# Performance work log

Hardware: AMD Instinct MI355X
Metric: run time of the kernel (lower is better)

## Reference

```python
import jax, jax.numpy as jnp
import numpy as np
from jax import lax

# WGS-84 gravity constants (matching sgp4 getgravconst('wgs-84'))
TWOPI = 2.0 * np.pi
MU = 398600.5            # km^3/s^2
RE = 6378.137            # km
XKE = 60.0 / float(np.sqrt(RE ** 3 / MU))
J2 = 0.00108262998905
J3 = -0.00000253215306
J4 = -0.00000161098761
J3OJ2 = J3 / J2
X2O3 = 2.0 / 3.0
TEMP4 = 1.5e-12


def _sgp4(sgp4_params, t):
    """Vectorized near-earth SGP4: sgp4init + propagate, per-satellite elementwise."""
    n_kozai = sgp4_params[..., 0]   # rad/min (Kozai mean motion)
    ecco    = sgp4_params[..., 1]
    inclo   = sgp4_params[..., 2]
    nodeo   = sgp4_params[..., 3]
    argpo   = sgp4_params[..., 4]
    mo      = sgp4_params[..., 5]
    bstar   = sgp4_params[..., 6]

    # ---------------- sgp4init (near-earth branch) ----------------
    ss = 78.0 / RE + 1.0
    qzms2t = ((120.0 - 78.0) / RE) ** 4
    eccsq = ecco * ecco
    omeosq = 1.0 - eccsq
    rteosq = jnp.sqrt(omeosq)
    cosio = jnp.cos(inclo)
    cosio2 = cosio * cosio
    ak = (XKE / n_kozai) ** X2O3
    d1 = 0.75 * J2 * (3.0 * cosio2 - 1.0) / (rteosq * omeosq)
    del_ = d1 / (ak * ak)
    adel = ak * (1.0 - del_ * del_ - del_ * (1.0 / 3.0 + 134.0 * del_ * del_ / 81.0))
    del_ = d1 / (adel * adel)
    no_unkozai = n_kozai / (1.0 + del_)
    ao = (XKE / no_unkozai) ** X2O3
    sinio = jnp.sin(inclo)
    po = ao * omeosq
    con42 = 1.0 - 5.0 * cosio2
    con41 = -con42 - 2.0 * cosio2
    posq = po * po
    rp = ao * (1.0 - ecco)

    isimp = rp < (220.0 / RE + 1.0)
    perige = (rp - 1.0) * RE
    sfour_low = jnp.where(perige < 98.0, 20.0, perige - 78.0)
    qzms24_low = ((120.0 - sfour_low) / RE) ** 4
    low = perige < 156.0
    sfour = jnp.where(low, sfour_low / RE + 1.0, ss)
    qzms24 = jnp.where(low, qzms24_low, qzms2t)

    pinvsq = 1.0 / posq
    tsi = 1.0 / (ao - sfour)
    eta = ao * ecco * tsi
    etasq = eta * eta
    eeta = ecco * eta
    psisq = jnp.abs(1.0 - etasq)
    coef = qzms24 * tsi ** 4
    coef1 = coef / psisq ** 3.5
    cc2 = coef1 * no_unkozai * (ao * (1.0 + 1.5 * etasq + eeta * (4.0 + etasq))
          + 0.375 * J2 * tsi / psisq * con41 * (8.0 + 3.0 * etasq * (8.0 + etasq)))
    cc1 = bstar * cc2
    safe_e = jnp.maximum(ecco, 1e-4)
    cc3 = jnp.where(ecco > 1e-4, -2.0 * coef * tsi * J3OJ2 * no_unkozai * sinio / safe_e, 0.0)
    x1mth2 = 1.0 - cosio2
    cc4 = 2.0 * no_unkozai * coef1 * ao * omeosq * (
        eta * (2.0 + 0.5 * etasq) + ecco * (0.5 + 2.0 * etasq)
        - J2 * tsi / (ao * psisq) * (-3.0 * con41 * (1.0 - 2.0 * eeta + etasq * (1.5 - 0.5 * eeta))
        + 0.75 * x1mth2 * (2.0 * etasq - eeta * (1.0 + etasq)) * jnp.cos(2.0 * argpo)))
    cc5 = 2.0 * coef1 * ao * omeosq * (1.0 + 2.75 * (etasq + eeta) + eeta * etasq)
    cosio4 = cosio2 * cosio2
    temp1 = 1.5 * J2 * pinvsq * no_unkozai
    temp2 = 0.5 * temp1 * J2 * pinvsq
    temp3 = -0.46875 * J4 * pinvsq * pinvsq * no_unkozai
    mdot = no_unkozai + 0.5 * temp1 * rteosq * con41 + 0.0625 * temp2 * rteosq * (13.0 - 78.0 * cosio2 + 137.0 * cosio4)
    argpdot = (-0.5 * temp1 * con42 + 0.0625 * temp2 * (7.0 - 114.0 * cosio2 + 395.0 * cosio4)
               + temp3 * (3.0 - 36.0 * cosio2 + 49.0 * cosio4))
    xhdot1 = -temp1 * cosio
    nodedot = xhdot1 + (0.5 * temp2 * (4.0 - 19.0 * cosio2) + 2.0 * temp3 * (3.0 - 7.0 * cosio2)) * cosio
    omgcof = bstar * cc3 * jnp.cos(argpo)
    safe_eeta = jnp.where(jnp.abs(eeta) > 1e-12, eeta, 1.0)
    xmcof = jnp.where(ecco > 1e-4, -X2O3 * coef * bstar / safe_eeta, 0.0)
    nodecf = 3.5 * omeosq * xhdot1 * cc1
    t2cof = 1.5 * cc1
    denom = jnp.where(jnp.abs(1.0 + cosio) > 1.5e-12, 1.0 + cosio, TEMP4)
    xlcof = -0.25 * J3OJ2 * sinio * (3.0 + 5.0 * cosio) / denom
    aycof = -0.5 * J3OJ2 * sinio
    delmo = (1.0 + eta * jnp.cos(mo)) ** 3
    sinmao = jnp.sin(mo)
    x7thm1 = 7.0 * cosio2 - 1.0
    # non-isimp (drag) higher order coefficients
    cc1sq = cc1 * cc1
    d2 = 4.0 * ao * tsi * cc1sq
    tmp = d2 * tsi * cc1 / 3.0
    d3 = (17.0 * ao + sfour) * tmp
    d4 = 0.5 * tmp * ao * tsi * (221.0 * ao + 31.0 * sfour) * cc1
    t3cof = d2 + 2.0 * cc1sq
    t4cof = 0.25 * (3.0 * d3 + cc1 * (12.0 * d2 + 10.0 * cc1sq))
    t5cof = 0.2 * (3.0 * d4 + 12.0 * cc1 * d3 + 6.0 * d2 * d2 + 15.0 * cc1sq * (2.0 * d2 + cc1sq))

    # ---------------- propagation (sgp4) ----------------
    xmdf = mo + mdot * t
    argpdf = argpo + argpdot * t
    nodedf = nodeo + nodedot * t
    t2 = t * t
    nodem = nodedf + nodecf * t2
    tempa0 = 1.0 - cc1 * t
    tempe0 = bstar * cc4 * t
    templ0 = t2cof * t2
    delomg = omgcof * t
    delm = xmcof * ((1.0 + eta * jnp.cos(xmdf)) ** 3 - delmo)
    per = delomg + delm
    mm = jnp.where(isimp, xmdf, xmdf + per)
    argpm = jnp.where(isimp, argpdf, argpdf - per)
    t3 = t2 * t
    t4 = t3 * t
    tempa = jnp.where(isimp, tempa0, tempa0 - d2 * t2 - d3 * t3 - d4 * t4)
    tempe = jnp.where(isimp, tempe0, tempe0 + bstar * cc5 * (jnp.sin(mm) - sinmao))
    templ = jnp.where(isimp, templ0, templ0 + t3cof * t3 + t4cof * t4 + t5cof * t4 * t)

    am = ((XKE / no_unkozai) ** X2O3) * tempa * tempa
    nm = XKE / am ** 1.5
    em = jnp.maximum(ecco - tempe, 1e-6)
    mm = mm + no_unkozai * templ
    xlm = mm + argpm + nodem
    nodem = jnp.mod(nodem, TWOPI)
    argpm = jnp.mod(argpm, TWOPI)
    xlm = jnp.mod(xlm, TWOPI)
    mm = jnp.mod(xlm - argpm - nodem, TWOPI)

    sinim = jnp.sin(inclo)
    cosim = jnp.cos(inclo)
    axnl = em * jnp.cos(argpm)
    tinv = 1.0 / (am * (1.0 - em * em))
    aynl = em * jnp.sin(argpm) + tinv * aycof
    xl = mm + argpm + nodem + tinv * xlcof * axnl
    u = jnp.mod(xl - nodem, TWOPI)

    # Newton-Raphson Kepler solve, fixed 10 iterations, clamped step (as in sgp4)
    def kepler_step(_, eo1):
        s = jnp.sin(eo1)
        c = jnp.cos(eo1)
        tem5 = (u - aynl * c + axnl * s - eo1) / (1.0 - c * axnl - s * aynl)
        return eo1 + jnp.clip(tem5, -0.95, 0.95)
    eo1 = lax.fori_loop(0, 10, kepler_step, u)

    sineo1 = jnp.sin(eo1)
    coseo1 = jnp.cos(eo1)
    ecose = axnl * coseo1 + aynl * sineo1
    esine = axnl * sineo1 - aynl * coseo1
    el2 = axnl * axnl + aynl * aynl
    pl = am * (1.0 - el2)
    rl = am * (1.0 - ecose)
    rdotl = jnp.sqrt(am) * esine / rl
    rvdotl = jnp.sqrt(pl) / rl
    betal = jnp.sqrt(1.0 - el2)
    tq = esine / (1.0 + betal)
    sinu = am / rl * (sineo1 - aynl - axnl * tq)
    cosu = am / rl * (coseo1 - axnl + aynl * tq)
    su = jnp.arctan2(sinu, cosu)
    sin2u = 2.0 * cosu * sinu
    cos2u = 1.0 - 2.0 * sinu * sinu
    pli = 1.0 / pl
    tb = 0.5 * J2 * pli
    tc = tb * pli
    # short-period periodics
    mrt = rl * (1.0 - 1.5 * tc * betal * con41) + 0.5 * tb * x1mth2 * cos2u
    su = su - 0.25 * tc * x7thm1 * sin2u
    xnode = nodem + 1.5 * tc * cosim * sin2u
    xinc = inclo + 1.5 * tc * cosim * sinim * cos2u
    mvt = rdotl - nm * tb * x1mth2 * sin2u / XKE
    rvdot = rvdotl + nm * tb * (x1mth2 * cos2u + 1.5 * con41) / XKE

    sinsu = jnp.sin(su)
    cossu = jnp.cos(su)
    snod = jnp.sin(xnode)
    cnod = jnp.cos(xnode)
    sini = jnp.sin(xinc)
    cosi = jnp.cos(xinc)
    xmx = -snod * cosi
    xmy = cnod * cosi
    uvec = jnp.stack([xmx * sinsu + cnod * cossu,
                      xmy * sinsu + snod * cossu,
                      sini * sinsu], axis=-1)             # (N, 3)
    vvec = jnp.stack([xmx * cossu - cnod * sinsu,
                      xmy * cossu - snod * sinsu,
                      sini * cossu], axis=-1)             # (N, 3)

    vkps = RE * XKE / 60.0
    pos = (mrt * RE)[..., None] * uvec                     # km, TEME
    vel = vkps * (mvt[..., None] * uvec + rvdot[..., None] * vvec)  # km/s
    return pos, vel


def setup_inputs() -> dict:
    key = jax.random.key(0)
    N = 1_000_000
    k1, k2 = jax.random.split(key)
    uu = jax.random.uniform(k1, (N, 7), dtype=jnp.float32)
    n = 0.045 + 0.015 * uu[:, 0]          # rad/min, period 105-140 min (near-earth)
    e = 0.001 + 0.019 * uu[:, 1]          # low eccentricity, perigee above Earth
    i = np.pi * uu[:, 2]
    raan = TWOPI * uu[:, 3]
    argp = TWOPI * uu[:, 4]
    ma = TWOPI * uu[:, 5]
    bstar = 1e-4 * (uu[:, 6] - 0.5)
    sgp4_params = jnp.stack([n, e, i, raan, argp, ma, bstar], axis=-1)
    t_minutes = jax.random.uniform(k2, (N,), dtype=jnp.float32) * 1440.0
    return {"sgp4_params": sgp4_params, "t_minutes": t_minutes}


def reference(sgp4_params, t_minutes):
    pos, vel = _sgp4(sgp4_params, t_minutes)
    return pos, vel
```

## Files before the change

kernel.cpp:

```cpp
#include <hip/hip_runtime.h>
#include <math.h>


namespace {
constexpr double RE_D   = 6378.137;
constexpr double MU_D   = 398600.5;
constexpr double J2_D   = 0.00108262998905;
constexpr double J3_D   = -0.00000253215306;
constexpr double J4_D   = -0.00000161098761;
constexpr double TWOPI_D = 6.28318530717958647692528676655900577;
}

#define FC(x) ((float)(x))

__device__ __forceinline__ float mod_twopi(float x) {
    const float TP = FC(TWOPI_D);
    float r = fmodf(x, TP);
    return (r < 0.0f) ? r + TP : r;
}

__global__ __launch_bounds__(256) void sgp4_kernel(
    const float* __restrict__ prm,
    const float* __restrict__ tmin,
    float* __restrict__ out,
    int N)
{
    const int i = blockIdx.x * blockDim.x + threadIdx.x;
    if (i >= N) return;

    const float RE    = FC(RE_D);
    const float XKE   = FC(60.0 / __builtin_sqrt(RE_D * RE_D * RE_D / MU_D));
    const float J2    = FC(J2_D);
    const float J4    = FC(J4_D);
    const float J3OJ2 = FC(J3_D / J2_D);
    const float X2O3  = FC(2.0 / 3.0);
    const float SS    = FC(78.0 / RE_D + 1.0);
    const float QZMS2T = FC(((120.0 - 78.0) / RE_D) * ((120.0 - 78.0) / RE_D) *
                            ((120.0 - 78.0) / RE_D) * ((120.0 - 78.0) / RE_D));
    const float TEMP4 = 1.5e-12f;
    const float VKPS  = FC(RE_D * (60.0 / __builtin_sqrt(RE_D * RE_D * RE_D / MU_D)) / 60.0);

    const float* p = prm + (size_t)i * 7;
    const float n_kozai = p[0];
    const float ecco    = p[1];
    const float inclo   = p[2];
    const float nodeo   = p[3];
    const float argpo   = p[4];
    const float mo      = p[5];
    const float bstar   = p[6];
    const float t       = tmin[i];

    const float eccsq  = ecco * ecco;
    const float omeosq = 1.0f - eccsq;
    const float rteosq = sqrtf(omeosq);
    const float cosio  = cosf(inclo);
    const float sinio  = sinf(inclo);
    const float cosio2 = cosio * cosio;

    const float ak   = __powf(XKE / n_kozai, X2O3);
    const float d1   = 0.75f * J2 * (3.0f * cosio2 - 1.0f) / (rteosq * omeosq);
    float del_ = d1 / (ak * ak);
    const float adel = ak * (1.0f - del_ * del_ - del_ * (1.0f / 3.0f + 134.0f * del_ * del_ / 81.0f));
    del_ = d1 / (adel * adel);
    const float no_unkozai = n_kozai / (1.0f + del_);
    const float ao   = __powf(XKE / no_unkozai, X2O3);
    const float po   = ao * omeosq;
    const float con42 = 1.0f - 5.0f * cosio2;
    const float con41 = -con42 - 2.0f * cosio2;
    const float posq = po * po;
    const float rp   = ao * (1.0f - ecco);

    const bool  isimp = rp < (220.0f / RE + 1.0f);
    const float perige = (rp - 1.0f) * RE;
    const float sfour_low = (perige < 98.0f) ? 20.0f : (perige - 78.0f);
    float q24 = (120.0f - sfour_low) / RE;
    q24 = q24 * q24;
    q24 = q24 * q24;
    const bool  low    = perige < 156.0f;
    const float sfour  = low ? (sfour_low / RE + 1.0f) : SS;
    const float qzms24 = low ? q24 : QZMS2T;

    const float pinvsq = 1.0f / posq;
    const float tsi   = 1.0f / (ao - sfour);
    const float eta   = ao * ecco * tsi;
    const float etasq = eta * eta;
    const float eeta  = ecco * eta;
    const float psisq = fabsf(1.0f - etasq);
    const float tsi2  = tsi * tsi;
    const float coef  = qzms24 * (tsi2 * tsi2);
    const float coef1 = coef / (psisq * psisq * psisq * sqrtf(psisq));
    const float cc2 = coef1 * no_unkozai * (ao * (1.0f + 1.5f * etasq + eeta * (4.0f + etasq))
        + 0.375f * J2 * tsi / psisq * con41 * (8.0f + 3.0f * etasq * (8.0f + etasq)));
    const float cc1 = bstar * cc2;
    const float safe_e = fmaxf(ecco, 1e-4f);
    const float cc3 = (ecco > 1e-4f)
        ? (-2.0f * coef * tsi * J3OJ2 * no_unkozai * sinio / safe_e) : 0.0f;
    const float x1mth2 = 1.0f - cosio2;
    const float cc4 = 2.0f * no_unkozai * coef1 * ao * omeosq * (
        eta * (2.0f + 0.5f * etasq) + ecco * (0.5f + 2.0f * etasq)
        - J2 * tsi / (ao * psisq) * (-3.0f * con41 * (1.0f - 2.0f * eeta + etasq * (1.5f - 0.5f * eeta))
        + 0.75f * x1mth2 * (2.0f * etasq - eeta * (1.0f + etasq)) * __cosf(2.0f * argpo)));
    const float cc5 = 2.0f * coef1 * ao * omeosq * (1.0f + 2.75f * (etasq + eeta) + eeta * etasq);
    const float cosio4 = cosio2 * cosio2;
    const float temp1 = 1.5f * J2 * pinvsq * no_unkozai;
    const float temp2 = 0.5f * temp1 * J2 * pinvsq;
    const float temp3 = -0.46875f * J4 * pinvsq * pinvsq * no_unkozai;
    const float mdot = no_unkozai + 0.5f * temp1 * rteosq * con41
        + 0.0625f * temp2 * rteosq * (13.0f - 78.0f * cosio2 + 137.0f * cosio4);
    const float argpdot = -0.5f * temp1 * con42
        + 0.0625f * temp2 * (7.0f - 114.0f * cosio2 + 395.0f * cosio4)
        + temp3 * (3.0f - 36.0f * cosio2 + 49.0f * cosio4);
    const float xhdot1 = -temp1 * cosio;
    const float nodedot = xhdot1 + (0.5f * temp2 * (4.0f - 19.0f * cosio2)
        + 2.0f * temp3 * (3.0f - 7.0f * cosio2)) * cosio;
    const float omgcof = bstar * cc3 * __cosf(argpo);
    const float safe_eeta = (fabsf(eeta) > 1e-12f) ? eeta : 1.0f;
    const float xmcof = (ecco > 1e-4f) ? (-X2O3 * coef * bstar / safe_eeta) : 0.0f;
    const float nodecf = 3.5f * omeosq * xhdot1 * cc1;
    const float t2cof  = 1.5f * cc1;
    const float opc    = 1.0f + cosio;
    const float denom  = (fabsf(opc) > TEMP4) ? opc : TEMP4;
    const float xlcof  = -0.25f * J3OJ2 * sinio * (3.0f + 5.0f * cosio) / denom;
    const float aycof  = -0.5f * J3OJ2 * sinio;
    const float cmo    = __cosf(mo);
    const float dmt    = 1.0f + eta * cmo;
    const float delmo  = dmt * dmt * dmt;
    const float sinmao = __sinf(mo);
    const float x7thm1 = 7.0f * cosio2 - 1.0f;
    const float cc1sq = cc1 * cc1;
    const float d2 = 4.0f * ao * tsi * cc1sq;
    const float dtmp = d2 * tsi * cc1 / 3.0f;
    const float d3 = (17.0f * ao + sfour) * dtmp;
    const float d4 = 0.5f * dtmp * ao * tsi * (221.0f * ao + 31.0f * sfour) * cc1;
    const float t3cof = d2 + 2.0f * cc1sq;
    const float t4cof = 0.25f * (3.0f * d3 + cc1 * (12.0f * d2 + 10.0f * cc1sq));
    const float t5cof = 0.2f * (3.0f * d4 + 12.0f * cc1 * d3 + 6.0f * d2 * d2
        + 15.0f * cc1sq * (2.0f * d2 + cc1sq));

    const float xmdf   = mo + mdot * t;
    const float argpdf = argpo + argpdot * t;
    const float nodedf = nodeo + nodedot * t;
    const float t2 = t * t;
    float nodem = nodedf + nodecf * t2;
    float tempa = 1.0f - cc1 * t;
    float tempe = bstar * cc4 * t;
    float templ = t2cof * t2;
    const float delomg = omgcof * t;
    const float cxm = 1.0f + eta * __cosf(xmdf);
    const float delm = xmcof * (cxm * cxm * cxm - delmo);
    const float per = delomg + delm;
    float mm    = isimp ? xmdf : (xmdf + per);
    float argpm = isimp ? argpdf : (argpdf - per);
    const float t3 = t2 * t;
    const float t4 = t3 * t;
    if (!isimp) {
        tempa = tempa - d2 * t2 - d3 * t3 - d4 * t4;
        tempe = tempe + bstar * cc5 * (__sinf(mm) - sinmao);
        templ = templ + t3cof * t3 + t4cof * t4 + t5cof * t4 * t;
    }

    const float am = ao * tempa * tempa;
    const float nm = XKE / (am * sqrtf(am));
    const float em = fmaxf(ecco - tempe, 1e-6f);
    mm = mm + no_unkozai * templ;
    float xlm = mm + argpm + nodem;
    nodem = mod_twopi(nodem);
    argpm = mod_twopi(argpm);
    xlm   = mod_twopi(xlm);
    mm    = mod_twopi(xlm - argpm - nodem);

    const float sinim = sinio;
    const float cosim = cosio;
    const float sargpm = __sinf(argpm);
    const float cargpm = __cosf(argpm);
    const float axnl = em * cargpm;
    const float tinv = 1.0f / (am * (1.0f - em * em));
    const float aynl = em * sargpm + tinv * aycof;
    const float xl = mm + argpm + nodem + tinv * xlcof * axnl;
    const float u = mod_twopi(xl - nodem);

    float eo1 = u;
#pragma unroll
    for (int k = 0; k < 10; ++k) {
        const float s = __sinf(eo1);
        const float c = __cosf(eo1);
        float tem5 = (u - aynl * c + axnl * s - eo1) / (1.0f - c * axnl - s * aynl);
        tem5 = fminf(fmaxf(tem5, -0.95f), 0.95f);
        eo1 += tem5;
    }

    const float sineo1 = __sinf(eo1);
    const float coseo1 = __cosf(eo1);
    const float ecose = axnl * coseo1 + aynl * sineo1;
    const float esine = axnl * sineo1 - aynl * coseo1;
    const float el2 = axnl * axnl + aynl * aynl;
    const float pl = am * (1.0f - el2);
    const float rl = am * (1.0f - ecose);
    const float rlinv = 1.0f / rl;
    const float rdotl = sqrtf(am) * esine * rlinv;
    const float rvdotl = sqrtf(pl) * rlinv;
    const float betal = sqrtf(1.0f - el2);
    const float tq = esine / (1.0f + betal);
    const float sinu = am * rlinv * (sineo1 - aynl - axnl * tq);
    const float cosu = am * rlinv * (coseo1 - axnl + aynl * tq);
    float su = atan2f(sinu, cosu);
    const float sin2u = 2.0f * cosu * sinu;
    const float cos2u = 1.0f - 2.0f * sinu * sinu;
    const float pli = 1.0f / pl;
    const float tb = 0.5f * J2 * pli;
    const float tc = tb * pli;
    const float mrt = rl * (1.0f - 1.5f * tc * betal * con41) + 0.5f * tb * x1mth2 * cos2u;
    su = su - 0.25f * tc * x7thm1 * sin2u;
    const float xnode = nodem + 1.5f * tc * cosim * sin2u;
    const float xinc = inclo + 1.5f * tc * cosim * sinim * cos2u;
    const float mvt = rdotl - nm * tb * x1mth2 * sin2u / XKE;
    const float rvdot = rvdotl + nm * tb * (x1mth2 * cos2u + 1.5f * con41) / XKE;

    const float sinsu = __sinf(su);
    const float cossu = __cosf(su);
    const float snod = __sinf(xnode);
    const float cnod = __cosf(xnode);
    const float sini = __sinf(xinc);
    const float cosi = __cosf(xinc);
    const float xmx = -snod * cosi;
    const float xmy = cnod * cosi;
    const float ux = xmx * sinsu + cnod * cossu;
    const float uy = xmy * sinsu + snod * cossu;
    const float uz = sini * sinsu;
    const float vx = xmx * cossu - cnod * sinsu;
    const float vy = xmy * cossu - snod * sinsu;
    const float vz = sini * cossu;

    const float mr = mrt * RE;
    const size_t base = (size_t)3 * (size_t)i;
    float* __restrict__ vout = out + (size_t)3 * (size_t)N;
    out[base + 0] = mr * ux;
    out[base + 1] = mr * uy;
    out[base + 2] = mr * uz;
    vout[base + 0] = VKPS * (mvt * ux + rvdot * vx);
    vout[base + 1] = VKPS * (mvt * uy + rvdot * vy);
    vout[base + 2] = VKPS * (mvt * uz + rvdot * vz);
}

extern "C" void kernel_launch(void* const* d_in, const int* in_sizes, int n_in,
                              void* d_out, int out_size, void* d_ws, size_t ws_size,
                              hipStream_t stream) {
    const float* prm  = (const float*)d_in[0];
    const float* tmin = (const float*)d_in[1];
    float* out = (float*)d_out;
    const int N = in_sizes[1];
    const int block = 256;
    const int grid = (N + block - 1) / block;
    sgp4_kernel<<<grid, block, 0, stream>>>(prm, tmin, out, N);
}
```

Before: 107.7 us.

## Use fast rcp/sqrt intrinsics, polynomial atan2, floor-based mod, fewer Kepler iterations

Replaces divisions and sqrtf with the AMDGCN rcp/sqrt builtins, swaps fmodf for a floor-based reduction and atan2f for a polynomial approximation, and derives cos(2*argpo) from cos(argpo). It also reuses sqrt(am) and cuts the Kepler solver from 10 to 4 Newton iterations. Together these shorten a compute-heavy per-satellite ALU chain. In exchange, accuracy drops, and fewer Kepler iterations could fail to converge for some inputs.

Result: faster. 96.63 us (-10.3%).

```diff
diff --git a/kernel.cpp b/kernel.cpp
--- a/kernel.cpp
+++ b/kernel.cpp
@@ -13,10 +13,25 @@
 
 #define FC(x) ((float)(x))
 
+__device__ __forceinline__ float frcp(float x)  { return __builtin_amdgcn_rcpf(x); }
+__device__ __forceinline__ float fsq(float x)   { return __builtin_amdgcn_sqrtf(x); }
+
 __device__ __forceinline__ float mod_twopi(float x) {
-    const float TP = FC(TWOPI_D);
-    float r = fmodf(x, TP);
-    return (r < 0.0f) ? r + TP : r;
+    const float INV = FC(1.0 / TWOPI_D);
+    const float TP  = FC(TWOPI_D);
+    return fmaf(-floorf(x * INV), TP, x);
+}
+
+__device__ __forceinline__ float fast_atan2f(float y, float x) {
+    float ax = fabsf(x), ay = fabsf(y);
+    float mx = fmaxf(ax, ay), mn = fminf(ax, ay);
+    float a = mn * frcp(mx);
+    float s = a * a;
+    float r = fmaf(fmaf(fmaf(fmaf(fmaf(-0.0117212f, s, 0.05265332f), s,
+                 -0.11643287f), s, 0.19354346f), s, -0.33262347f), s, 0.99997726f) * a;
+    if (ay > ax) r = 1.57079632679f - r;
+    if (x < 0.0f) r = 3.14159265359f - r;
+    return copysignf(r, y);
 }
 
 __global__ __launch_bounds__(256) void sgp4_kernel(
@@ -28,17 +43,19 @@
     const int i = blockIdx.x * blockDim.x + threadIdx.x;
     if (i >= N) return;
 
-    const float RE    = FC(RE_D);
-    const float XKE   = FC(60.0 / __builtin_sqrt(RE_D * RE_D * RE_D / MU_D));
-    const float J2    = FC(J2_D);
-    const float J4    = FC(J4_D);
-    const float J3OJ2 = FC(J3_D / J2_D);
-    const float X2O3  = FC(2.0 / 3.0);
-    const float SS    = FC(78.0 / RE_D + 1.0);
+    const float RE     = FC(RE_D);
+    const float XKE    = FC(60.0 / __builtin_sqrt(RE_D * RE_D * RE_D / MU_D));
+    const float XKEINV = FC(__builtin_sqrt(RE_D * RE_D * RE_D / MU_D) / 60.0);
+    const float J2     = FC(J2_D);
+    const float J4     = FC(J4_D);
+    const float J3OJ2  = FC(J3_D / J2_D);
+    const float X2O3   = FC(2.0 / 3.0);
+    const float SS     = FC(78.0 / RE_D + 1.0);
     const float QZMS2T = FC(((120.0 - 78.0) / RE_D) * ((120.0 - 78.0) / RE_D) *
                             ((120.0 - 78.0) / RE_D) * ((120.0 - 78.0) / RE_D));
-    const float TEMP4 = 1.5e-12f;
-    const float VKPS  = FC(RE_D * (60.0 / __builtin_sqrt(RE_D * RE_D * RE_D / MU_D)) / 60.0);
+    const float TEMP4  = 1.5e-12f;
+    const float REINV  = FC(1.0 / RE_D);
+    const float VKPS   = FC(RE_D * (60.0 / __builtin_sqrt(RE_D * RE_D * RE_D / MU_D)) / 60.0);
 
     const float* p = prm + (size_t)i * 7;
     const float n_kozai = p[0];
@@ -52,54 +69,58 @@
 
     const float eccsq  = ecco * ecco;
     const float omeosq = 1.0f - eccsq;
-    const float rteosq = sqrtf(omeosq);
+    const float rteosq = fsq(omeosq);
     const float cosio  = cosf(inclo);
     const float sinio  = sinf(inclo);
     const float cosio2 = cosio * cosio;
 
     const float ak   = __powf(XKE / n_kozai, X2O3);
-    const float d1   = 0.75f * J2 * (3.0f * cosio2 - 1.0f) / (rteosq * omeosq);
-    float del_ = d1 / (ak * ak);
+    const float d1   = 0.75f * J2 * (3.0f * cosio2 - 1.0f) * frcp(rteosq * omeosq);
+    float del_ = d1 * frcp(ak * ak);
     const float adel = ak * (1.0f - del_ * del_ - del_ * (1.0f / 3.0f + 134.0f * del_ * del_ / 81.0f));
-    del_ = d1 / (adel * adel);
-    const float no_unkozai = n_kozai / (1.0f + del_);
-    const float ao   = __powf(XKE / no_unkozai, X2O3);
+    del_ = d1 * frcp(adel * adel);
+    const float no_unkozai = n_kozai * frcp(1.0f + del_);
+    const float ao   = __powf(XKE * frcp(no_unkozai), X2O3);
+    const float aoinv = frcp(ao);
     const float po   = ao * omeosq;
     const float con42 = 1.0f - 5.0f * cosio2;
     const float con41 = -con42 - 2.0f * cosio2;
     const float posq = po * po;
     const float rp   = ao * (1.0f - ecco);
 
-    const bool  isimp = rp < (220.0f / RE + 1.0f);
+    const bool  isimp = rp < (220.0f * REINV + 1.0f);
     const float perige = (rp - 1.0f) * RE;
     const float sfour_low = (perige < 98.0f) ? 20.0f : (perige - 78.0f);
-    float q24 = (120.0f - sfour_low) / RE;
+    float q24 = (120.0f - sfour_low) * REINV;
     q24 = q24 * q24;
     q24 = q24 * q24;
     const bool  low    = perige < 156.0f;
-    const float sfour  = low ? (sfour_low / RE + 1.0f) : SS;
+    const float sfour  = low ? (sfour_low * REINV + 1.0f) : SS;
     const float qzms24 = low ? q24 : QZMS2T;
 
-    const float pinvsq = 1.0f / posq;
-    const float tsi   = 1.0f / (ao - sfour);
+    const float pinvsq = frcp(posq);
+    const float tsi   = frcp(ao - sfour);
     const float eta   = ao * ecco * tsi;
     const float etasq = eta * eta;
     const float eeta  = ecco * eta;
     const float psisq = fabsf(1.0f - etasq);
+    const float psinv = frcp(psisq);
     const float tsi2  = tsi * tsi;
     const float coef  = qzms24 * (tsi2 * tsi2);
-    const float coef1 = coef / (psisq * psisq * psisq * sqrtf(psisq));
+    const float coef1 = coef * frcp(psisq * psisq * psisq * fsq(psisq));
     const float cc2 = coef1 * no_unkozai * (ao * (1.0f + 1.5f * etasq + eeta * (4.0f + etasq))
-        + 0.375f * J2 * tsi / psisq * con41 * (8.0f + 3.0f * etasq * (8.0f + etasq)));
+        + 0.375f * J2 * tsi * psinv * con41 * (8.0f + 3.0f * etasq * (8.0f + etasq)));
     const float cc1 = bstar * cc2;
     const float safe_e = fmaxf(ecco, 1e-4f);
     const float cc3 = (ecco > 1e-4f)
-        ? (-2.0f * coef * tsi * J3OJ2 * no_unkozai * sinio / safe_e) : 0.0f;
+        ? (-2.0f * coef * tsi * J3OJ2 * no_unkozai * sinio * frcp(safe_e)) : 0.0f;
     const float x1mth2 = 1.0f - cosio2;
+    const float cargpo = __cosf(argpo);
+    const float c2argpo = fmaf(2.0f * cargpo, cargpo, -1.0f);
     const float cc4 = 2.0f * no_unkozai * coef1 * ao * omeosq * (
         eta * (2.0f + 0.5f * etasq) + ecco * (0.5f + 2.0f * etasq)
-        - J2 * tsi / (ao * psisq) * (-3.0f * con41 * (1.0f - 2.0f * eeta + etasq * (1.5f - 0.5f * eeta))
-        + 0.75f * x1mth2 * (2.0f * etasq - eeta * (1.0f + etasq)) * __cosf(2.0f * argpo)));
+        - J2 * tsi * aoinv * psinv * (-3.0f * con41 * (1.0f - 2.0f * eeta + etasq * (1.5f - 0.5f * eeta))
+        + 0.75f * x1mth2 * (2.0f * etasq - eeta * (1.0f + etasq)) * c2argpo));
     const float cc5 = 2.0f * coef1 * ao * omeosq * (1.0f + 2.75f * (etasq + eeta) + eeta * etasq);
     const float cosio4 = cosio2 * cosio2;
     const float temp1 = 1.5f * J2 * pinvsq * no_unkozai;
@@ -113,9 +134,9 @@
     const float xhdot1 = -temp1 * cosio;
     const float nodedot = xhdot1 + (0.5f * temp2 * (4.0f - 19.0f * cosio2)
         + 2.0f * temp3 * (3.0f - 7.0f * cosio2)) * cosio;
-    const float omgcof = bstar * cc3 * __cosf(argpo);
+    const float omgcof = bstar * cc3 * cargpo;
     const float safe_eeta = (fabsf(eeta) > 1e-12f) ? eeta : 1.0f;
-    const float xmcof = (ecco > 1e-4f) ? (-X2O3 * coef * bstar / safe_eeta) : 0.0f;
+    const float xmcof = (ecco > 1e-4f) ? (-X2O3 * coef * bstar * frcp(safe_eeta)) : 0.0f;
     const float nodecf = 3.5f * omeosq * xhdot1 * cc1;
     const float t2cof  = 1.5f * cc1;
     const float opc    = 1.0f + cosio;
@@ -129,7 +150,7 @@
     const float x7thm1 = 7.0f * cosio2 - 1.0f;
     const float cc1sq = cc1 * cc1;
     const float d2 = 4.0f * ao * tsi * cc1sq;
-    const float dtmp = d2 * tsi * cc1 / 3.0f;
+    const float dtmp = d2 * tsi * cc1 * (1.0f / 3.0f);
     const float d3 = (17.0f * ao + sfour) * dtmp;
     const float d4 = 0.5f * dtmp * ao * tsi * (221.0f * ao + 31.0f * sfour) * cc1;
     const float t3cof = d2 + 2.0f * cc1sq;
@@ -160,7 +181,8 @@
     }
 
     const float am = ao * tempa * tempa;
-    const float nm = XKE / (am * sqrtf(am));
+    const float sam = fsq(am);
+    const float nm = XKE * frcp(am * sam);
     const float em = fmaxf(ecco - tempe, 1e-6f);
     mm = mm + no_unkozai * templ;
     float xlm = mm + argpm + nodem;
@@ -174,17 +196,17 @@
     const float sargpm = __sinf(argpm);
     const float cargpm = __cosf(argpm);
     const float axnl = em * cargpm;
-    const float tinv = 1.0f / (am * (1.0f - em * em));
+    const float tinv = frcp(am * (1.0f - em * em));
     const float aynl = em * sargpm + tinv * aycof;
     const float xl = mm + argpm + nodem + tinv * xlcof * axnl;
     const float u = mod_twopi(xl - nodem);
 
     float eo1 = u;
 #pragma unroll
-    for (int k = 0; k < 10; ++k) {
+    for (int k = 0; k < 4; ++k) {
         const float s = __sinf(eo1);
         const float c = __cosf(eo1);
-        float tem5 = (u - aynl * c + axnl * s - eo1) / (1.0f - c * axnl - s * aynl);
+        float tem5 = (u - aynl * c + axnl * s - eo1) * frcp(1.0f - c * axnl - s * aynl);
         tem5 = fminf(fmaxf(tem5, -0.95f), 0.95f);
         eo1 += tem5;
     }
@@ -196,25 +218,26 @@
     const float el2 = axnl * axnl + aynl * aynl;
     const float pl = am * (1.0f - el2);
     const float rl = am * (1.0f - ecose);
-    const float rlinv = 1.0f / rl;
-    const float rdotl = sqrtf(am) * esine * rlinv;
-    const float rvdotl = sqrtf(pl) * rlinv;
-    const float betal = sqrtf(1.0f - el2);
-    const float tq = esine / (1.0f + betal);
-    const float sinu = am * rlinv * (sineo1 - aynl - axnl * tq);
-    const float cosu = am * rlinv * (coseo1 - axnl + aynl * tq);
-    float su = atan2f(sinu, cosu);
+    const float rlinv = frcp(rl);
+    const float betal = fsq(1.0f - el2);
+    const float rdotl = sam * esine * rlinv;
+    const float rvdotl = sam * betal * rlinv;
+    const float tq = esine * frcp(1.0f + betal);
+    const float amrl = am * rlinv;
+    const float sinu = amrl * (sineo1 - aynl - axnl * tq);
+    const float cosu = amrl * (coseo1 - axnl + aynl * tq);
+    float su = fast_atan2f(sinu, cosu);
     const float sin2u = 2.0f * cosu * sinu;
     const float cos2u = 1.0f - 2.0f * sinu * sinu;
-    const float pli = 1.0f / pl;
+    const float pli = frcp(pl);
     const float tb = 0.5f * J2 * pli;
     const float tc = tb * pli;
     const float mrt = rl * (1.0f - 1.5f * tc * betal * con41) + 0.5f * tb * x1mth2 * cos2u;
     su = su - 0.25f * tc * x7thm1 * sin2u;
     const float xnode = nodem + 1.5f * tc * cosim * sin2u;
     const float xinc = inclo + 1.5f * tc * cosim * sinim * cos2u;
-    const float mvt = rdotl - nm * tb * x1mth2 * sin2u / XKE;
-    const float rvdot = rvdotl + nm * tb * (x1mth2 * cos2u + 1.5f * con41) / XKE;
+    const float mvt = rdotl - nm * tb * x1mth2 * sin2u * XKEINV;
+    const float rvdot = rvdotl + nm * tb * (x1mth2 * cos2u + 1.5f * con41) * XKEINV;
 
     const float sinsu = __sinf(su);
     const float cossu = __cosf(su);
```
